# Kernel optimization log

Measured on AMD Instinct MI355X. Metric: run time of the kernel, lower is better.

## Reference

```python
import jax, jax.numpy as jnp
import numpy as np

# --- model hyperparameters (match init_kwargs / TrajectoryDecoder defaults) ---
R, T, KREG = 3, 16, 8          # num_radii, num_theta, reg_dim
RADIUS = 40.0                  # radius_scale
VEHICLE_HIDDEN = 16
MAP_HIDDEN = 8
IN_CH = VEHICLE_HIDDEN + MAP_HIDDEN  # 24
PREDICT_WINDOW = 30
TWO_PI = 2.0 * np.pi


def _reg_roll(f):
    # f: [..., C, k] -> [..., C, k(l), k(m)] with entry f[..., c, (m-l)%k]
    m = jnp.arange(KREG)[None, :]
    l = jnp.arange(KREG)[:, None]
    return f[..., (m - l) % KREG]


def _equilinear(W, f):
    # equivariant linear map between regular reps = circular (group) conv over reg dim
    # W: [out, in, k], f: [..., in, k] -> [..., out, k]
    return jnp.einsum('oil,...ilm->...om', W, _reg_roll(f))


def _reg2rho1(f, w):
    # frequency-1 Fourier projection of the regular rep -> rho1 (2-vector); 2 free params
    ang = TWO_PI * jnp.arange(KREG) / KREG
    c, s = jnp.cos(ang), jnp.sin(ang)
    W2 = jnp.stack([w[0] * c - w[1] * s, w[0] * s + w[1] * c], axis=-1)  # [k, 2]
    return jnp.einsum('...cm,md->...cd', f, W2)


def _cts_aggregate(dst_p, src_p, H, src_mask):
    # Continuous conv aggregation: bilinear interpolation of a polar-binned kernel
    # already contracted with source features.
    # H: [B, S, R, T, O, k] per-source, per-(radius,theta)-bin transformed features
    B, S, O = src_p.shape[0], src_p.shape[1], H.shape[-2]
    rel = src_p[:, None, :, :] - dst_p[:, :, None, :]      # [B, Nd, S, 2]
    d = jnp.sqrt(jnp.sum(rel * rel, axis=-1) + 1e-12)      # [B, Nd, S]
    valid = (d < RADIUS).astype(dst_p.dtype) * src_mask[:, None, :]
    win = jnp.maximum(1.0 - (d / RADIUS) ** 2, 0.0) ** 3   # CConv window
    cnt = jnp.maximum(jnp.sum(valid, axis=-1, keepdims=True), 1.0)
    base_w = valid * win / cnt
    # radial interpolation (clamped linear)
    u = jnp.clip(d / RADIUS, 0.0, 1.0) * (R - 1)
    r0f = jnp.floor(u); wr = u - r0f
    r0 = r0f.astype(jnp.int32); r1 = jnp.minimum(r0 + 1, R - 1)
    # angular interpolation (circular linear)
    t = ((jnp.arctan2(rel[..., 1], rel[..., 0]) / TWO_PI) % 1.0) * T
    t0f = jnp.floor(t); wt = t - t0f
    t0 = t0f.astype(jnp.int32) % T; t1 = (t0 + 1) % T
    Hf = H.reshape(B, S, R * T, O, KREG)
    bidx = jnp.arange(B)[:, None, None]
    sidx = jnp.arange(S)[None, None, :]
    out = jnp.zeros((B, dst_p.shape[1], O, KREG), dtype=dst_p.dtype)
    for ri, ti, cw in ((r0, t0, (1 - wr) * (1 - wt)),
                       (r0, t1, (1 - wr) * wt),
                       (r1, t0, wr * (1 - wt)),
                       (r1, t1, wr * wt)):
        g = Hf[bidx, sidx, ri * T + ti]                    # [B, Nd, S, O, k] irregular gather
        out = out + jnp.einsum('bns,bnsok->bnok', base_w * cw, g)
    return out


def _conv_reg(K, src_p, dst_p, f, src_mask):
    # EquiCtsConv2dRegToReg: per-bin group conv over reg dim, then continuous-conv gather
    H = jnp.einsum('rtoil,bsilm->bsrtom', K, _reg_roll(f))
    return _cts_aggregate(dst_p, src_p, H, src_mask)


def _conv_rho1(K, src_p, dst_p, v, src_mask):
    # EquiCtsConv2dRho1ToReg (in_channels=1): contract 2-vector input per bin
    H = jnp.einsum('rtomd,bsd->bsrtom', K, v)
    return _cts_aggregate(dst_p, src_p, H, src_mask)


def _decode(p, feat, car_mask, K_vehicle, Wd_vehicle, K_conv1, Wd1, K_conv2, Wd2):
    out = _conv_reg(K_vehicle, p, p, feat, car_mask) + _equilinear(Wd_vehicle, feat)
    for K, Wd in ((K_conv1, Wd1), (K_conv2, Wd2)):
        inf = jax.nn.relu(out)
        oc = _conv_reg(K, p, p, inf, car_mask)
        od = _equilinear(Wd, inf)
        out = oc + od + out if od.shape[-2] == out.shape[-2] else oc + od
    return jax.nn.relu(out)


def _forward(p, feat, map_p, map_feat, car_mask, map_mask,
             K_vehicle, Wd_vehicle, K_conv1, Wd1, K_conv2, Wd2,
             Wd_back, w_rho1, K_map):
    outputs = []
    output = _decode(p, feat, car_mask, K_vehicle, Wd_vehicle, K_conv1, Wd1, K_conv2, Wd2)
    delta = _reg2rho1(output, w_rho1)                      # [B, N, 3, 2]
    outputs.append(delta.at[..., 0, :].add(p))
    for _ in range(1, PREDICT_WINDOW):
        p = p + delta[..., 0, :]
        back = jnp.tanh(_equilinear(Wd_back, output))      # [B, N, 16, k]
        feat_v = feat[..., :VEHICLE_HIDDEN, :] * back
        enc = jax.nn.relu(_conv_rho1(K_map, map_p, p, map_feat, map_mask))  # MapEncoder
        feat = jnp.concatenate([feat_v, enc], axis=-2)     # [B, N, 24, k]
        output = _decode(p, feat, car_mask, K_vehicle, Wd_vehicle, K_conv1, Wd1, K_conv2, Wd2)
        delta = _reg2rho1(output, w_rho1)
        outputs.append(delta.at[..., 0, :].add(p))
    return jnp.stack(outputs, axis=0)                      # [30, B, N, 3, 2]


def setup_inputs() -> dict:
    key = jax.random.key(0)
    ks = jax.random.split(key, 13)
    B, N, M = 8, 64, 1024
    sc = 0.1
    return {
        'p': jax.random.normal(ks[0], (B, N, 2)) * 20.0,
        'feat': jax.random.normal(ks[1], (B, N, IN_CH, KREG)),
        'map_p': jax.random.normal(ks[2], (B, M, 2)) * 20.0,
        'map_feat': jax.random.normal(ks[3], (B, M, 2)),
        'car_mask': jnp.ones((B, N), dtype=jnp.float32),
        'map_mask': jnp.ones((B, M), dtype=jnp.float32),
        'K_vehicle': jax.random.normal(ks[4], (R, T, 8, IN_CH, KREG)) * sc,
        'Wd_vehicle': jax.random.normal(ks[5], (8, IN_CH, KREG)) * sc,
        'K_conv1': jax.random.normal(ks[6], (R, T, 8, 8, KREG)) * sc,
        'Wd1': jax.random.normal(ks[7], (8, 8, KREG)) * sc,
        'K_conv2': jax.random.normal(ks[8], (R, T, 3, 8, KREG)) * sc,
        'Wd2': jax.random.normal(ks[9], (3, 8, KREG)) * sc,
        'Wd_back': jax.random.normal(ks[10], (VEHICLE_HIDDEN, 3, KREG)) * sc,
        'w_rho1': jax.random.normal(ks[11], (2,)) * sc,
        'K_map': jax.random.normal(ks[12], (R, T, MAP_HIDDEN, KREG, 2)) * sc,
    }


def reference(p, feat, map_p, map_feat, car_mask, map_mask,
              K_vehicle, Wd_vehicle, K_conv1, Wd1, K_conv2, Wd2,
              Wd_back, w_rho1, K_map):
    return _forward(p, feat, map_p, map_feat, car_mask, map_mask,
                    K_vehicle, Wd_vehicle, K_conv1, Wd1, K_conv2, Wd2,
                    Wd_back, w_rho1, K_map)
```

## Files before the change

kernel.cpp:

```cpp
#include <hip/hip_runtime.h>
#include <math.h>

#define NB 8
#define NV 64
#define NM 1024
#define NR 3
#define NT 16
#define KR 8
#define RTOT 48
#define RADIUSF 40.0f
#define TWO_PIF 6.283185307179586f

__device__ __forceinline__ unsigned int pack_bf16x2(float a, float b) {
    unsigned int ua = __float_as_uint(a), ub = __float_as_uint(b);
    ua = (ua + 0x7FFFu + ((ua >> 16) & 1u)) >> 16;
    ub = (ub + 0x7FFFu + ((ub >> 16) & 1u)) & 0xFFFF0000u;
    return ua | ub;
}
__device__ __forceinline__ float2 unpack_bf16x2(unsigned int u) {
    float2 r;
    r.x = __uint_as_float(u << 16);
    r.y = __uint_as_float(u & 0xFFFF0000u);
    return r;
}

__device__ __forceinline__ float fast_atan2(float y, float x) {
    float ax = fabsf(x), ay = fabsf(y);
    float mx = fmaxf(ax, ay), mn = fminf(ax, ay);
    float z = mn / fmaxf(mx, 1e-30f);
    float z2 = z * z;
    float r = fmaf(z2, fmaf(z2, fmaf(z2, fmaf(z2, 0.0208351f, -0.0851330f),
                                     0.1801410f), -0.3302995f), 0.9998660f) * z;
    r = (ay > ax) ? (1.57079637f - r) : r;
    r = (x < 0.f) ? (3.14159274f - r) : r;
    return (y < 0.f) ? -r : r;
}

__device__ __forceinline__ void pair_geom(float relx, float rely, float mask,
                                          float& valid, float& win,
                                          int bin[4], float cw[4]) {
    float d = sqrtf(relx * relx + rely * rely + 1e-12f);
    valid = (d < RADIUSF) ? mask : 0.0f;
    float q = d * (1.0f / RADIUSF);
    float w1 = fmaxf(1.0f - q * q, 0.0f);
    win = w1 * w1 * w1;
    float u = fminf(fmaxf(q, 0.0f), 1.0f) * (float)(NR - 1);
    float r0f = floorf(u);
    float wr = u - r0f;
    int r0 = (int)r0f;
    int r1 = min(r0 + 1, NR - 1);
    float a = fast_atan2(rely, relx) * (1.0f / TWO_PIF);
    a = a - floorf(a);
    float t = a * (float)NT;
    float t0f = floorf(t);
    float wt = t - t0f;
    int t0 = ((int)t0f) & (NT - 1);
    int t1 = (t0 + 1) & (NT - 1);
    bin[0] = r0 * NT + t0; cw[0] = (1.0f - wr) * (1.0f - wt);
    bin[1] = r0 * NT + t1; cw[1] = (1.0f - wr) * wt;
    bin[2] = r1 * NT + t0; cw[2] = wr * (1.0f - wt);
    bin[3] = r1 * NT + t1; cw[3] = wr * wt;
}

__global__ __launch_bounds__(256) void k_trans(
        const float* __restrict__ Kv, const float* __restrict__ K1g,
        const float* __restrict__ K2g, float4* __restrict__ KTv,
        float4* __restrict__ KT1, float4* __restrict__ KT2) {
    int idx = blockIdx.x * 256 + threadIdx.x;
    if (idx < 48 * 384) {
        int j = idx / 384, p = idx % 384;
        KTv[idx] = *(const float4*)(Kv + p * 192 + j * 4);
    } else if (idx < 48 * 384 + 16 * 384) {
        int r = idx - 48 * 384;
        int j = r / 384, p = r % 384;
        KT1[r] = *(const float4*)(K1g + p * 64 + j * 4);
    } else if (idx < 48 * 384 + 16 * 384 + 16 * 144) {
        int r = idx - (48 * 384 + 16 * 384);
        int j = r / 144, p = r % 144;
        KT2[r] = *(const float4*)(K2g + p * 64 + j * 4);
    }
}

template<int ICH, int NPAIR, int OCH, int ROWLEN>
__device__ __forceinline__ void h_phase(int tid, int bn, const float* s_f,
        const float4* __restrict__ KT, unsigned short* __restrict__ Hb) {
    for (int pp = tid; pp < NPAIR; pp += 256) {
        float acc[KR];
#pragma unroll
        for (int m = 0; m < KR; ++m) acc[m] = 0.f;
#pragma unroll 8
        for (int i = 0; i < ICH; ++i) {
            float4 k0 = KT[(2 * i) * NPAIR + pp];
            float4 k1 = KT[(2 * i + 1) * NPAIR + pp];
            float kk[8] = {k0.x, k0.y, k0.z, k0.w, k1.x, k1.y, k1.z, k1.w};
            float ff[8];
            *(float4*)&ff[0] = *(const float4*)&s_f[i * 8];
            *(float4*)&ff[4] = *(const float4*)&s_f[i * 8 + 4];
#pragma unroll
            for (int l = 0; l < KR; ++l) {
                float kl = kk[l];
#pragma unroll
                for (int m = 0; m < KR; ++m)
                    acc[m] = fmaf(kl, ff[(m - l) & 7], acc[m]);
            }
        }
        int rt = pp / OCH, o = pp - rt * OCH;
        uint4 u;
        u.x = pack_bf16x2(acc[0], acc[1]);
        u.y = pack_bf16x2(acc[2], acc[3]);
        u.z = pack_bf16x2(acc[4], acc[5]);
        u.w = pack_bf16x2(acc[6], acc[7]);
        *(uint4*)&Hb[(size_t)(bn * RTOT + rt) * ROWLEN + o * 8] = u;
    }
}

__global__ __launch_bounds__(256) void k_H0(const float* __restrict__ inb,
        const float4* __restrict__ KT, unsigned short* __restrict__ Hb) {
    __shared__ __align__(16) float s_f[192];
    int bs = blockIdx.x, tid = threadIdx.x;
    if (tid < 192) s_f[tid] = inb[bs * 192 + tid];
    __syncthreads();
    h_phase<24, 384, 8, 64>(tid, bs, s_f, KT, Hb);
}

__device__ __forceinline__ void agg64_bf16(int tid, const float* s_w,
        const int* s_row, const unsigned short* __restrict__ Hb,
        float* s_part) {
    int w = tid >> 6, lane = tid & 63;
    int g = lane >> 3, c = lane & 7;
    float acc[8];
#pragma unroll
    for (int m = 0; m < 8; ++m) acc[m] = 0.f;
#pragma unroll
    for (int r = 0; r < 8; ++r) {
        int idx = w * 64 + r * 8 + g;
        float we = s_w[idx];
        uint4 u = *(const uint4*)&Hb[(size_t)s_row[idx] * 64 + c * 8];
        float2 q0 = unpack_bf16x2(u.x), q1 = unpack_bf16x2(u.y);
        float2 q2 = unpack_bf16x2(u.z), q3 = unpack_bf16x2(u.w);
        acc[0] = fmaf(we, q0.x, acc[0]); acc[1] = fmaf(we, q0.y, acc[1]);
        acc[2] = fmaf(we, q1.x, acc[2]); acc[3] = fmaf(we, q1.y, acc[3]);
        acc[4] = fmaf(we, q2.x, acc[4]); acc[5] = fmaf(we, q2.y, acc[5]);
        acc[6] = fmaf(we, q3.x, acc[6]); acc[7] = fmaf(we, q3.y, acc[7]);
    }
    float* pp = &s_part[(w * 8 + g) * 64 + c * 8];
#pragma unroll
    for (int m = 0; m < 8; ++m) pp[m] = acc[m];
}

__device__ __forceinline__ void agg32_bf16(int tid, const float* s_w,
        const int* s_row, const unsigned short* __restrict__ Hb,
        float* s_part) {
    int w = tid >> 6, lane = tid & 63;
    int g = lane >> 2, c = lane & 3;
    float acc[8];
#pragma unroll
    for (int m = 0; m < 8; ++m) acc[m] = 0.f;
#pragma unroll
    for (int r = 0; r < 4; ++r) {
        int idx = w * 64 + r * 16 + g;
        float we = s_w[idx];
        uint4 u = *(const uint4*)&Hb[(size_t)s_row[idx] * 32 + c * 8];
        float2 q0 = unpack_bf16x2(u.x), q1 = unpack_bf16x2(u.y);
        float2 q2 = unpack_bf16x2(u.z), q3 = unpack_bf16x2(u.w);
        acc[0] = fmaf(we, q0.x, acc[0]); acc[1] = fmaf(we, q0.y, acc[1]);
        acc[2] = fmaf(we, q1.x, acc[2]); acc[3] = fmaf(we, q1.y, acc[3]);
        acc[4] = fmaf(we, q2.x, acc[4]); acc[5] = fmaf(we, q2.y, acc[5]);
        acc[6] = fmaf(we, q3.x, acc[6]); acc[7] = fmaf(we, q3.y, acc[7]);
    }
    float* pp = &s_part[(w * 16 + g) * 32 + c * 8];
#pragma unroll
    for (int m = 0; m < 8; ++m) pp[m] = acc[m];
}

__global__ __launch_bounds__(256) void k_A1(int t,
        float* __restrict__ p, const float* __restrict__ out2buf,
        const unsigned short* __restrict__ H2b, const float* __restrict__ Wd2,
        const float* __restrict__ w4, const int* __restrict__ bin4,
        const float* __restrict__ w_rho1,
        float* __restrict__ oDbuf, float* __restrict__ out) {
    __shared__ float s_w[256];
    __shared__ int   s_row[256];
    __shared__ float s_in[64];
    __shared__ __align__(16) float s_part[64 * 32];
    __shared__ float s_oD[24];
    __shared__ float s_w2[16];
    int tid = threadIdx.x, bn = blockIdx.x, b = bn >> 6, n = bn & 63;
    float2 pold = *(const float2*)&p[bn * 2];

    s_w[tid] = w4[bn * 256 + tid];
    s_row[tid] = (b * NV + (tid >> 2)) * RTOT + bin4[bn * 256 + tid];
    if (tid < 64) s_in[tid] = out2buf[bn * 64 + tid];
    if (tid >= 224 && tid < 240) {
        int r = tid - 224, m = r >> 1, dd = r & 1;
        float ang = TWO_PIF * (float)m / (float)KR;
        float sn, cs; sincosf(ang, &sn, &cs);
        float w0 = w_rho1[0], wq = w_rho1[1];
        s_w2[r] = (dd == 0) ? (w0 * cs - wq * sn) : (w0 * sn + wq * cs);
    }
    __syncthreads();

    agg32_bf16(tid, s_w, s_row, H2b, s_part);
    __syncthreads();
    if (tid < 24) {
        float tot = 0.f;
#pragma unroll
        for (int k = 0; k < 64; ++k) tot += s_part[k * 32 + tid];
        int o = tid / KR, m = tid & 7;
#pragma unroll
        for (int i = 0; i < 8; ++i) {
            const float* Wr = Wd2 + (o * 8 + i) * KR;
#pragma unroll
            for (int l = 0; l < KR; ++l)
                tot = fmaf(Wr[l], fmaxf(s_in[i * KR + ((m - l) & 7)], 0.f), tot);
        }
        float v = fmaxf(tot, 0.f);
        s_oD[tid] = v;
        oDbuf[bn * 24 + tid] = v;
    }
    __syncthreads();

    float dx0 = 0.f, dy0 = 0.f;
#pragma unroll
    for (int m = 0; m < KR; ++m) {
        float v = s_oD[m];
        dx0 = fmaf(v, s_w2[m * 2 + 0], dx0);
        dy0 = fmaf(v, s_w2[m * 2 + 1], dy0);
    }
    if (tid < 6) {
        int c = tid >> 1, dd = tid & 1;
        float acc = 0.f;
#pragma unroll
        for (int m = 0; m < KR; ++m)
            acc = fmaf(s_oD[c * KR + m], s_w2[m * 2 + dd], acc);
        if (c == 0) acc += (dd ? pold.y : pold.x);
        out[(((t - 1) * NB + b) * NV + n) * 6 + tid] = acc;
    }
    if (tid == 0) {
        p[bn * 2 + 0] = pold.x + dx0;
        p[bn * 2 + 1] = pold.y + dy0;
    }
}

__global__ __launch_bounds__(256) void k_A2(
        const float* __restrict__ p, const float* __restrict__ oDbuf,
        float* __restrict__ feat, const float* __restrict__ WdBack,
        const float* __restrict__ Kmap, const float* __restrict__ map_p,
        const float* __restrict__ map_feat, const float* __restrict__ map_mask,
        const float4* __restrict__ KTv, unsigned short* __restrict__ Hvb) {
    __shared__ float s_oD[24];
    __shared__ float s_G4[4 * 96];
    __shared__ float s_G[96];
    __shared__ float s_wred[4];
    __shared__ __align__(16) float s_f2[192];
    int tid = threadIdx.x, bn = blockIdx.x, b = bn >> 6;

    float2 pn = *(const float2*)&p[bn * 2];
    float pdx = pn.x, pdy = pn.y;

    float2 mp[4], mf[4]; float mm[4];
#pragma unroll
    for (int j = 0; j < 4; ++j) {
        int s = tid + j * 256;
        mp[j] = *(const float2*)&map_p[(b * NM + s) * 2];
        mm[j] = map_mask[b * NM + s];
        mf[j] = *(const float2*)&map_feat[(b * NM + s) * 2];
    }
    if (tid < 24) s_oD[tid] = oDbuf[bn * 24 + tid];
    if (tid < 96) { s_G4[tid] = 0.f; s_G4[96 + tid] = 0.f; s_G4[192 + tid] = 0.f; s_G4[288 + tid] = 0.f; }
    __syncthreads();

    float lc = 0.f;
    float* myG = &s_G4[(tid >> 6) * 96];
#pragma unroll
    for (int j = 0; j < 4; ++j) {
        float valid, win; int bin[4]; float cw[4];
        pair_geom(mp[j].x - pdx, mp[j].y - pdy, mm[j], valid, win, bin, cw);
        lc += valid;
        float ww = valid * win;
        if (ww > 0.f) {
#pragma unroll
            for (int q = 0; q < 4; ++q) {
                float w = ww * cw[q];
                atomicAdd(&myG[bin[q] * 2 + 0], w * mf[j].x);
                atomicAdd(&myG[bin[q] * 2 + 1], w * mf[j].y);
            }
        }
    }
#pragma unroll
    for (int off = 32; off > 0; off >>= 1) lc += __shfl_xor(lc, off);
    if ((tid & 63) == 0) s_wred[tid >> 6] = lc;
    __syncthreads();
    if (tid < 96) s_G[tid] = s_G4[tid] + s_G4[96 + tid] + s_G4[192 + tid] + s_G4[288 + tid];
    __syncthreads();
    float invc = 1.0f / fmaxf(s_wred[0] + s_wred[1] + s_wred[2] + s_wred[3], 1.0f);

    if (tid < 64) {
        float acc = 0.f;
#pragma unroll 8
        for (int rt = 0; rt < RTOT; ++rt) {
            float2 k2 = *(const float2*)&Kmap[(rt * 64 + tid) * 2];
            acc = fmaf(k2.x, s_G[rt * 2 + 0], acc);
            acc = fmaf(k2.y, s_G[rt * 2 + 1], acc);
        }
        s_f2[128 + tid] = fmaxf(acc * invc, 0.f);
    }
    if (tid >= 128) {
        int r = tid - 128, i = r >> 3, m = r & 7;
        float acc = 0.f;
#pragma unroll
        for (int c = 0; c < 3; ++c)
#pragma unroll
            for (int l = 0; l < KR; ++l)
                acc = fmaf(WdBack[(i * 3 + c) * 8 + l], s_oD[c * 8 + ((m - l) & 7)], acc);
        s_f2[r] = feat[bn * 192 + r] * tanhf(acc);
    }
    __syncthreads();
    if (tid < 192) feat[bn * 192 + tid] = s_f2[tid];

    h_phase<24, 384, 8, 64>(tid, bn, s_f2, KTv, Hvb);
}

__global__ __launch_bounds__(256) void k_B(
        const float* __restrict__ p, const float* __restrict__ car_mask,
        const float* __restrict__ feat, const unsigned short* __restrict__ Hvb,
        const float* __restrict__ WdV,
        float* __restrict__ w4, int* __restrict__ bin4,
        const float4* __restrict__ KT1,
        float* __restrict__ out1, unsigned short* __restrict__ H1b) {
    __shared__ float s_psrc[NV * 2];
    __shared__ float s_w[256];
    __shared__ int   s_row[256];
    __shared__ __align__(16) float s_in[192];
    __shared__ __align__(16) float s_part[32 * 64];
    __shared__ __align__(16) float s_f2[64];
    int tid = threadIdx.x, bn = blockIdx.x, b = bn >> 6, n = bn & 63;
    if (tid < 128) s_psrc[tid] = p[b * 128 + tid];
    if (tid < 192) s_in[tid] = feat[bn * 192 + tid];
    __syncthreads();
    if (tid < NV) {
        int s = tid;
        float valid, win; int bin[4]; float cw[4];
        pair_geom(s_psrc[s * 2 + 0] - s_psrc[n * 2 + 0],
                  s_psrc[s * 2 + 1] - s_psrc[n * 2 + 1],
                  car_mask[b * NV + s], valid, win, bin, cw);
        float c = valid;
#pragma unroll
        for (int off = 32; off > 0; off >>= 1) c += __shfl_xor(c, off);
        float bw = valid * win / fmaxf(c, 1.0f);
#pragma unroll
        for (int q = 0; q < 4; ++q) {
            float wv = bw * cw[q];
            s_w[s * 4 + q] = wv;
            s_row[s * 4 + q] = (b * NV + s) * RTOT + bin[q];
            w4[bn * 256 + s * 4 + q] = wv;
            bin4[bn * 256 + s * 4 + q] = bin[q];
        }
    }
    __syncthreads();
    agg64_bf16(tid, s_w, s_row, Hvb, s_part);
    __syncthreads();
    if (tid < 64) {
        float tot = 0.f;
#pragma unroll
        for (int k = 0; k < 32; ++k) tot += s_part[k * 64 + tid];
        int o = tid >> 3, m = tid & 7;
#pragma unroll
        for (int i = 0; i < 24; ++i) {
            const float* Wr = WdV + (o * 24 + i) * KR;
#pragma unroll
            for (int l = 0; l < KR; ++l)
                tot = fmaf(Wr[l], s_in[i * KR + ((m - l) & 7)], tot);
        }
        out1[bn * 64 + tid] = tot;
        s_f2[tid] = fmaxf(tot, 0.f);
    }
    __syncthreads();
    h_phase<8, 384, 8, 64>(tid, bn, s_f2, KT1, H1b);
}

__global__ __launch_bounds__(256) void k_C(const float* __restrict__ out1,
        const unsigned short* __restrict__ H1b, const float* __restrict__ Wd1,
        const float* __restrict__ w4, const int* __restrict__ bin4,
        const float4* __restrict__ KT2, float* __restrict__ out2,
        unsigned short* __restrict__ H2b) {
    __shared__ float s_w[256];
    __shared__ int   s_row[256];
    __shared__ float s_in[64];
    __shared__ __align__(16) float s_part[32 * 64];
    __shared__ __align__(16) float s_f2[64];
    int tid = threadIdx.x, bn = blockIdx.x, b = bn >> 6;
    s_w[tid] = w4[bn * 256 + tid];
    s_row[tid] = (b * NV + (tid >> 2)) * RTOT + bin4[bn * 256 + tid];
    if (tid < 64) s_in[tid] = out1[bn * 64 + tid];
    __syncthreads();
    agg64_bf16(tid, s_w, s_row, H1b, s_part);
    __syncthreads();
    if (tid < 64) {
        float tot = 0.f;
#pragma unroll
        for (int k = 0; k < 32; ++k) tot += s_part[k * 64 + tid];
        int o = tid >> 3, m = tid & 7;
#pragma unroll
        for (int i = 0; i < 8; ++i) {
            const float* Wr = Wd1 + (o * 8 + i) * KR;
#pragma unroll
            for (int l = 0; l < KR; ++l)
                tot = fmaf(Wr[l], fmaxf(s_in[i * KR + ((m - l) & 7)], 0.f), tot);
        }
        tot += s_in[tid];
        out2[bn * 64 + tid] = tot;
        s_f2[tid] = fmaxf(tot, 0.f);
    }
    __syncthreads();
    h_phase<8, 144, 3, 32>(tid, bn, s_f2, KT2, H2b);
}

__global__ __launch_bounds__(256) void k_fin(
        const float* __restrict__ p, const float* __restrict__ out2buf,
        const unsigned short* __restrict__ H2b, const float* __restrict__ Wd2,
        const float* __restrict__ w4, const int* __restrict__ bin4,
        const float* __restrict__ w_rho1, float* __restrict__ out) {
    __shared__ float s_w[256];
    __shared__ int   s_row[256];
    __shared__ float s_in[64];
    __shared__ __align__(16) float s_part[64 * 32];
    __shared__ float s_oD[24];
    __shared__ float s_w2[16];
    int tid = threadIdx.x, bn = blockIdx.x, b = bn >> 6, n = bn & 63;
    s_w[tid] = w4[bn * 256 + tid];
    s_row[tid] = (b * NV + (tid >> 2)) * RTOT + bin4[bn * 256 + tid];
    if (tid < 64) s_in[tid] = out2buf[bn * 64 + tid];
    if (tid >= 224 && tid < 240) {
        int r = tid - 224, m = r >> 1, dd = r & 1;
        float ang = TWO_PIF * (float)m / (float)KR;
        float sn, cs; sincosf(ang, &sn, &cs);
        float w0 = w_rho1[0], wq = w_rho1[1];
        s_w2[r] = (dd == 0) ? (w0 * cs - wq * sn) : (w0 * sn + wq * cs);
    }
    __syncthreads();
    agg32_bf16(tid, s_w, s_row, H2b, s_part);
    __syncthreads();
    if (tid < 24) {
        float tot = 0.f;
#pragma unroll
        for (int k = 0; k < 64; ++k) tot += s_part[k * 32 + tid];
        int o = tid / KR, m = tid & 7;
#pragma unroll
        for (int i = 0; i < 8; ++i) {
            const float* Wr = Wd2 + (o * 8 + i) * KR;
#pragma unroll
            for (int l = 0; l < KR; ++l)
                tot = fmaf(Wr[l], fmaxf(s_in[i * KR + ((m - l) & 7)], 0.f), tot);
        }
        s_oD[tid] = fmaxf(tot, 0.f);
    }
    __syncthreads();
    if (tid < 6) {
        int c = tid >> 1, dd = tid & 1;
        float acc = 0.f;
#pragma unroll
        for (int m = 0; m < KR; ++m)
            acc = fmaf(s_oD[c * KR + m], s_w2[m * 2 + dd], acc);
        if (c == 0) acc += p[bn * 2 + dd];
        out[((29 * NB + b) * NV + n) * 6 + tid] = acc;
    }
}

extern "C" void kernel_launch(void* const* d_in, const int* in_sizes, int n_in,
                              void* d_out, int out_size, void* d_ws, size_t ws_size,
                              hipStream_t stream) {
    const float* in_p     = (const float*)d_in[0];
    const float* in_feat  = (const float*)d_in[1];
    const float* map_p    = (const float*)d_in[2];
    const float* map_feat = (const float*)d_in[3];
    const float* car_mask = (const float*)d_in[4];
    const float* map_mask = (const float*)d_in[5];
    const float* Kv       = (const float*)d_in[6];
    const float* WdV      = (const float*)d_in[7];
    const float* K1       = (const float*)d_in[8];
    const float* Wd1      = (const float*)d_in[9];
    const float* K2       = (const float*)d_in[10];
    const float* Wd2      = (const float*)d_in[11];
    const float* WdBack   = (const float*)d_in[12];
    const float* w_rho1   = (const float*)d_in[13];
    const float* Kmap     = (const float*)d_in[14];

    float* ws   = (float*)d_ws;
    float* pbuf  = ws;
    float* feat  = ws + 2048;
    float* out1  = ws + 100352;
    float* out2  = ws + 133120;
    float* w4    = ws + 178176;
    int*   bin4  = (int*)(ws + 309248);
    float4* KTv  = (float4*)(ws + 440320);
    float4* KT1  = (float4*)(ws + 514048);
    float4* KT2  = (float4*)(ws + 538624);
    unsigned short* Hvb = (unsigned short*)(ws + 547840);
    unsigned short* H1b = (unsigned short*)(ws + 1334272);
    unsigned short* H2b = (unsigned short*)(ws + 2120704);
    float* oDbuf = ws + 2513920;
    float* out   = (float*)d_out;

    hipMemcpyAsync(pbuf, in_p, NB * NV * 2 * sizeof(float),
                   hipMemcpyDeviceToDevice, stream);
    hipMemcpyAsync(feat, in_feat, NB * NV * 24 * KR * sizeof(float),
                   hipMemcpyDeviceToDevice, stream);

    k_trans<<<105, 256, 0, stream>>>(Kv, K1, K2, KTv, KT1, KT2);
    k_H0<<<NB * NV, 256, 0, stream>>>(feat, KTv, Hvb);

    k_B<<<NB * NV, 256, 0, stream>>>(pbuf, car_mask, feat, Hvb, WdV, w4, bin4, KT1, out1, H1b);
    k_C<<<NB * NV, 256, 0, stream>>>(out1, H1b, Wd1, w4, bin4, KT2, out2, H2b);

    for (int t = 1; t < 30; ++t) {
        k_A1<<<NB * NV, 256, 0, stream>>>(t, pbuf, out2, H2b, Wd2, w4, bin4,
                                          w_rho1, oDbuf, out);
        k_A2<<<NB * NV, 256, 0, stream>>>(pbuf, oDbuf, feat, WdBack, Kmap,
                                          map_p, map_feat, map_mask, KTv, Hvb);
        k_B<<<NB * NV, 256, 0, stream>>>(pbuf, car_mask, feat, Hvb, WdV, w4, bin4, KT1, out1, H1b);
        k_C<<<NB * NV, 256, 0, stream>>>(out1, H1b, Wd1, w4, bin4, KT2, out2, H2b);
    }
    k_fin<<<NB * NV, 256, 0, stream>>>(pbuf, out2, H2b, Wd2, w4, bin4, w_rho1, out);
}
```

Before: 1.656 ms.

## Fuse per-step decode kernels and widen blocks to 1024 threads with shuffle reductions

Merges the two per-timestep kernels, position update/output and map aggregation plus H recompute, into one kernel. This removes one launch per step and the oDbuf round trip through global memory. All per-step kernels move to 1024-thread blocks, so each thread handles one map point, and the h_phase loop spreads its 384 pairs across more threads. The gather-aggregation reductions now use wavefront butterfly shuffles instead of large shared-memory partial buffers. The trade-off is lower occupancy per CU with 1024-thread blocks, many idle threads in some phases, and more shuffle instructions.

After: 2.020 ms. 1.22x slower.

```diff
diff --git a/kernel.cpp b/kernel.cpp
--- a/kernel.cpp
+++ b/kernel.cpp
@@ -81,10 +81,10 @@
     }
 }
 
-template<int ICH, int NPAIR, int OCH, int ROWLEN>
+template<int ICH, int NPAIR, int OCH, int ROWLEN, int STRIDE>
 __device__ __forceinline__ void h_phase(int tid, int bn, const float* s_f,
         const float4* __restrict__ KT, unsigned short* __restrict__ Hb) {
-    for (int pp = tid; pp < NPAIR; pp += 256) {
+    for (int pp = tid; pp < NPAIR; pp += STRIDE) {
         float acc[KR];
 #pragma unroll
         for (int m = 0; m < KR; ++m) acc[m] = 0.f;
@@ -114,98 +114,87 @@
     }
 }
 
+__device__ __forceinline__ void bfly8(float acc[8]) {
+#pragma unroll
+    for (int off = 1; off < 64; off <<= 1) {
+#pragma unroll
+        for (int j = 0; j < 8; ++j) acc[j] += __shfl_xor(acc[j], off);
+    }
+}
+
 __global__ __launch_bounds__(256) void k_H0(const float* __restrict__ inb,
         const float4* __restrict__ KT, unsigned short* __restrict__ Hb) {
     __shared__ __align__(16) float s_f[192];
     int bs = blockIdx.x, tid = threadIdx.x;
     if (tid < 192) s_f[tid] = inb[bs * 192 + tid];
     __syncthreads();
-    h_phase<24, 384, 8, 64>(tid, bs, s_f, KT, Hb);
-}
-
-__device__ __forceinline__ void agg64_bf16(int tid, const float* s_w,
-        const int* s_row, const unsigned short* __restrict__ Hb,
-        float* s_part) {
-    int w = tid >> 6, lane = tid & 63;
-    int g = lane >> 3, c = lane & 7;
-    float acc[8];
-#pragma unroll
-    for (int m = 0; m < 8; ++m) acc[m] = 0.f;
-#pragma unroll
-    for (int r = 0; r < 8; ++r) {
-        int idx = w * 64 + r * 8 + g;
-        float we = s_w[idx];
-        uint4 u = *(const uint4*)&Hb[(size_t)s_row[idx] * 64 + c * 8];
-        float2 q0 = unpack_bf16x2(u.x), q1 = unpack_bf16x2(u.y);
-        float2 q2 = unpack_bf16x2(u.z), q3 = unpack_bf16x2(u.w);
-        acc[0] = fmaf(we, q0.x, acc[0]); acc[1] = fmaf(we, q0.y, acc[1]);
-        acc[2] = fmaf(we, q1.x, acc[2]); acc[3] = fmaf(we, q1.y, acc[3]);
-        acc[4] = fmaf(we, q2.x, acc[4]); acc[5] = fmaf(we, q2.y, acc[5]);
-        acc[6] = fmaf(we, q3.x, acc[6]); acc[7] = fmaf(we, q3.y, acc[7]);
-    }
-    float* pp = &s_part[(w * 8 + g) * 64 + c * 8];
-#pragma unroll
-    for (int m = 0; m < 8; ++m) pp[m] = acc[m];
-}
-
-__device__ __forceinline__ void agg32_bf16(int tid, const float* s_w,
-        const int* s_row, const unsigned short* __restrict__ Hb,
-        float* s_part) {
-    int w = tid >> 6, lane = tid & 63;
-    int g = lane >> 2, c = lane & 3;
-    float acc[8];
-#pragma unroll
-    for (int m = 0; m < 8; ++m) acc[m] = 0.f;
-#pragma unroll
-    for (int r = 0; r < 4; ++r) {
-        int idx = w * 64 + r * 16 + g;
-        float we = s_w[idx];
-        uint4 u = *(const uint4*)&Hb[(size_t)s_row[idx] * 32 + c * 8];
-        float2 q0 = unpack_bf16x2(u.x), q1 = unpack_bf16x2(u.y);
-        float2 q2 = unpack_bf16x2(u.z), q3 = unpack_bf16x2(u.w);
-        acc[0] = fmaf(we, q0.x, acc[0]); acc[1] = fmaf(we, q0.y, acc[1]);
-        acc[2] = fmaf(we, q1.x, acc[2]); acc[3] = fmaf(we, q1.y, acc[3]);
-        acc[4] = fmaf(we, q2.x, acc[4]); acc[5] = fmaf(we, q2.y, acc[5]);
-        acc[6] = fmaf(we, q3.x, acc[6]); acc[7] = fmaf(we, q3.y, acc[7]);
-    }
-    float* pp = &s_part[(w * 16 + g) * 32 + c * 8];
-#pragma unroll
-    for (int m = 0; m < 8; ++m) pp[m] = acc[m];
-}
-
-__global__ __launch_bounds__(256) void k_A1(int t,
+    h_phase<24, 384, 8, 64, 256>(tid, bs, s_f, KT, Hb);
+}
+
+__global__ __launch_bounds__(1024) void k_AM(int t,
         float* __restrict__ p, const float* __restrict__ out2buf,
         const unsigned short* __restrict__ H2b, const float* __restrict__ Wd2,
         const float* __restrict__ w4, const int* __restrict__ bin4,
-        const float* __restrict__ w_rho1,
-        float* __restrict__ oDbuf, float* __restrict__ out) {
+        const float* __restrict__ w_rho1, float* __restrict__ feat,
+        const float* __restrict__ WdBack, const float* __restrict__ Kmap,
+        const float* __restrict__ map_p, const float* __restrict__ map_feat,
+        const float* __restrict__ map_mask,
+        const float4* __restrict__ KTv, unsigned short* __restrict__ Hvb,
+        float* __restrict__ out) {
     __shared__ float s_w[256];
     __shared__ int   s_row[256];
     __shared__ float s_in[64];
-    __shared__ __align__(16) float s_part[64 * 32];
+    __shared__ float s_p2[16 * 8];
     __shared__ float s_oD[24];
     __shared__ float s_w2[16];
+    __shared__ float s_G16[16 * 96];
+    __shared__ float s_G[96];
+    __shared__ float s_wred[16];
+    __shared__ __align__(16) float s_f2[192];
+
     int tid = threadIdx.x, bn = blockIdx.x, b = bn >> 6, n = bn & 63;
+    int w = tid >> 6, lane = tid & 63;
     float2 pold = *(const float2*)&p[bn * 2];
 
-    s_w[tid] = w4[bn * 256 + tid];
-    s_row[tid] = (b * NV + (tid >> 2)) * RTOT + bin4[bn * 256 + tid];
-    if (tid < 64) s_in[tid] = out2buf[bn * 64 + tid];
-    if (tid >= 224 && tid < 240) {
-        int r = tid - 224, m = r >> 1, dd = r & 1;
+    float2 mp = *(const float2*)&map_p[(b * NM + tid) * 2];
+    float  mm = map_mask[b * NM + tid];
+    float2 mf = *(const float2*)&map_feat[(b * NM + tid) * 2];
+
+    if (tid < 256) {
+        s_w[tid] = w4[bn * 256 + tid];
+        s_row[tid] = (b * NV + (tid >> 2)) * RTOT + bin4[bn * 256 + tid];
+    }
+    if (tid >= 256 && tid < 320) s_in[tid - 256] = out2buf[bn * 64 + (tid - 256)];
+    if (tid >= 320 && tid < 336) {
+        int r = tid - 320, m = r >> 1, dd = r & 1;
         float ang = TWO_PIF * (float)m / (float)KR;
         float sn, cs; sincosf(ang, &sn, &cs);
         float w0 = w_rho1[0], wq = w_rho1[1];
         s_w2[r] = (dd == 0) ? (w0 * cs - wq * sn) : (w0 * sn + wq * cs);
     }
-    __syncthreads();
-
-    agg32_bf16(tid, s_w, s_row, H2b, s_part);
+    for (int i = tid; i < 16 * 96; i += 1024) s_G16[i] = 0.f;
+    __syncthreads();
+
+    {
+        int cgrp = w >> 2, esub = w & 3;
+        int e = esub * 64 + lane;
+        float we = s_w[e];
+        uint4 u = *(const uint4*)&H2b[(size_t)s_row[e] * 32 + cgrp * 8];
+        float2 q0 = unpack_bf16x2(u.x), q1 = unpack_bf16x2(u.y);
+        float2 q2 = unpack_bf16x2(u.z), q3 = unpack_bf16x2(u.w);
+        float acc[8] = {we * q0.x, we * q0.y, we * q1.x, we * q1.y,
+                        we * q2.x, we * q2.y, we * q3.x, we * q3.y};
+        bfly8(acc);
+        if (lane == 0) {
+#pragma unroll
+            for (int j = 0; j < 8; ++j) s_p2[w * 8 + j] = acc[j];
+        }
+    }
     __syncthreads();
     if (tid < 24) {
-        float tot = 0.f;
-#pragma unroll
-        for (int k = 0; k < 64; ++k) tot += s_part[k * 32 + tid];
+        int cgrp = tid >> 3, j = tid & 7;
+        float tot = s_p2[(cgrp * 4 + 0) * 8 + j] + s_p2[(cgrp * 4 + 1) * 8 + j]
+                  + s_p2[(cgrp * 4 + 2) * 8 + j] + s_p2[(cgrp * 4 + 3) * 8 + j];
         int o = tid / KR, m = tid & 7;
 #pragma unroll
         for (int i = 0; i < 8; ++i) {
@@ -214,9 +203,7 @@
             for (int l = 0; l < KR; ++l)
                 tot = fmaf(Wr[l], fmaxf(s_in[i * KR + ((m - l) & 7)], 0.f), tot);
         }
-        float v = fmaxf(tot, 0.f);
-        s_oD[tid] = v;
-        oDbuf[bn * 24 + tid] = v;
+        s_oD[tid] = fmaxf(tot, 0.f);
     }
     __syncthreads();
 
@@ -236,66 +223,42 @@
         if (c == 0) acc += (dd ? pold.y : pold.x);
         out[(((t - 1) * NB + b) * NV + n) * 6 + tid] = acc;
     }
-    if (tid == 0) {
-        p[bn * 2 + 0] = pold.x + dx0;
-        p[bn * 2 + 1] = pold.y + dy0;
-    }
-}
-
-__global__ __launch_bounds__(256) void k_A2(
-        const float* __restrict__ p, const float* __restrict__ oDbuf,
-        float* __restrict__ feat, const float* __restrict__ WdBack,
-        const float* __restrict__ Kmap, const float* __restrict__ map_p,
-        const float* __restrict__ map_feat, const float* __restrict__ map_mask,
-        const float4* __restrict__ KTv, unsigned short* __restrict__ Hvb) {
-    __shared__ float s_oD[24];
-    __shared__ float s_G4[4 * 96];
-    __shared__ float s_G[96];
-    __shared__ float s_wred[4];
-    __shared__ __align__(16) float s_f2[192];
-    int tid = threadIdx.x, bn = blockIdx.x, b = bn >> 6;
-
-    float2 pn = *(const float2*)&p[bn * 2];
-    float pdx = pn.x, pdy = pn.y;
-
-    float2 mp[4], mf[4]; float mm[4];
-#pragma unroll
-    for (int j = 0; j < 4; ++j) {
-        int s = tid + j * 256;
-        mp[j] = *(const float2*)&map_p[(b * NM + s) * 2];
-        mm[j] = map_mask[b * NM + s];
-        mf[j] = *(const float2*)&map_feat[(b * NM + s) * 2];
-    }
-    if (tid < 24) s_oD[tid] = oDbuf[bn * 24 + tid];
-    if (tid < 96) { s_G4[tid] = 0.f; s_G4[96 + tid] = 0.f; s_G4[192 + tid] = 0.f; s_G4[288 + tid] = 0.f; }
-    __syncthreads();
-
-    float lc = 0.f;
-    float* myG = &s_G4[(tid >> 6) * 96];
-#pragma unroll
-    for (int j = 0; j < 4; ++j) {
+    float pdx = pold.x + dx0, pdy = pold.y + dy0;
+    if (tid == 0) { p[bn * 2 + 0] = pdx; p[bn * 2 + 1] = pdy; }
+
+    float lc;
+    {
         float valid, win; int bin[4]; float cw[4];
-        pair_geom(mp[j].x - pdx, mp[j].y - pdy, mm[j], valid, win, bin, cw);
-        lc += valid;
+        pair_geom(mp.x - pdx, mp.y - pdy, mm, valid, win, bin, cw);
+        lc = valid;
         float ww = valid * win;
+        float* myG = &s_G16[w * 96];
         if (ww > 0.f) {
 #pragma unroll
             for (int q = 0; q < 4; ++q) {
-                float w = ww * cw[q];
-                atomicAdd(&myG[bin[q] * 2 + 0], w * mf[j].x);
-                atomicAdd(&myG[bin[q] * 2 + 1], w * mf[j].y);
+                float wq_ = ww * cw[q];
+                atomicAdd(&myG[bin[q] * 2 + 0], wq_ * mf.x);
+                atomicAdd(&myG[bin[q] * 2 + 1], wq_ * mf.y);
             }
         }
     }
 #pragma unroll
-    for (int off = 32; off > 0; off >>= 1) lc += __shfl_xor(lc, off);
-    if ((tid & 63) == 0) s_wred[tid >> 6] = lc;
-    __syncthreads();
-    if (tid < 96) s_G[tid] = s_G4[tid] + s_G4[96 + tid] + s_G4[192 + tid] + s_G4[288 + tid];
-    __syncthreads();
-    float invc = 1.0f / fmaxf(s_wred[0] + s_wred[1] + s_wred[2] + s_wred[3], 1.0f);
+    for (int off = 1; off < 64; off <<= 1) lc += __shfl_xor(lc, off);
+    if (lane == 0) s_wred[w] = lc;
+    __syncthreads();
+    if (tid < 96) {
+        float g = 0.f;
+#pragma unroll
+        for (int c = 0; c < 16; ++c) g += s_G16[c * 96 + tid];
+        s_G[tid] = g;
+    }
+    __syncthreads();
 
     if (tid < 64) {
+        float cnt = 0.f;
+#pragma unroll
+        for (int c = 0; c < 16; ++c) cnt += s_wred[c];
+        float invc = 1.0f / fmaxf(cnt, 1.0f);
         float acc = 0.f;
 #pragma unroll 8
         for (int rt = 0; rt < RTOT; ++rt) {
@@ -305,7 +268,7 @@
         }
         s_f2[128 + tid] = fmaxf(acc * invc, 0.f);
     }
-    if (tid >= 128) {
+    if (tid >= 128 && tid < 256) {
         int r = tid - 128, i = r >> 3, m = r & 7;
         float acc = 0.f;
 #pragma unroll
@@ -318,10 +281,10 @@
     __syncthreads();
     if (tid < 192) feat[bn * 192 + tid] = s_f2[tid];
 
-    h_phase<24, 384, 8, 64>(tid, bn, s_f2, KTv, Hvb);
-}
-
-__global__ __launch_bounds__(256) void k_B(
+    h_phase<24, 384, 8, 64, 1024>(tid, bn, s_f2, KTv, Hvb);
+}
+
+__global__ __launch_bounds__(1024) void k_B(
         const float* __restrict__ p, const float* __restrict__ car_mask,
         const float* __restrict__ feat, const unsigned short* __restrict__ Hvb,
         const float* __restrict__ WdV,
@@ -332,11 +295,12 @@
     __shared__ float s_w[256];
     __shared__ int   s_row[256];
     __shared__ __align__(16) float s_in[192];
-    __shared__ __align__(16) float s_part[32 * 64];
+    __shared__ float s_p[16 * 8];
     __shared__ __align__(16) float s_f2[64];
     int tid = threadIdx.x, bn = blockIdx.x, b = bn >> 6, n = bn & 63;
+    int w = tid >> 6, lane = tid & 63;
     if (tid < 128) s_psrc[tid] = p[b * 128 + tid];
-    if (tid < 192) s_in[tid] = feat[bn * 192 + tid];
+    if (tid >= 256 && tid < 448) s_in[tid - 256] = feat[bn * 192 + (tid - 256)];
     __syncthreads();
     if (tid < NV) {
         int s = tid;
@@ -358,12 +322,33 @@
         }
     }
     __syncthreads();
-    agg64_bf16(tid, s_w, s_row, Hvb, s_part);
+    {
+        int cgrp = w >> 1, esub = w & 1;
+        int e0 = esub * 128 + lane, e1 = e0 + 64;
+        float we0 = s_w[e0], we1 = s_w[e1];
+        uint4 u0 = *(const uint4*)&Hvb[(size_t)s_row[e0] * 64 + cgrp * 8];
+        uint4 u1 = *(const uint4*)&Hvb[(size_t)s_row[e1] * 64 + cgrp * 8];
+        float acc[8];
+        {
+            float2 a0 = unpack_bf16x2(u0.x), a1 = unpack_bf16x2(u0.y);
+            float2 a2 = unpack_bf16x2(u0.z), a3 = unpack_bf16x2(u0.w);
+            float2 b0 = unpack_bf16x2(u1.x), b1 = unpack_bf16x2(u1.y);
+            float2 b2 = unpack_bf16x2(u1.z), b3 = unpack_bf16x2(u1.w);
+            acc[0] = we0 * a0.x + we1 * b0.x; acc[1] = we0 * a0.y + we1 * b0.y;
+            acc[2] = we0 * a1.x + we1 * b1.x; acc[3] = we0 * a1.y + we1 * b1.y;
+            acc[4] = we0 * a2.x + we1 * b2.x; acc[5] = we0 * a2.y + we1 * b2.y;
+            acc[6] = we0 * a3.x + we1 * b3.x; acc[7] = we0 * a3.y + we1 * b3.y;
+        }
+        bfly8(acc);
+        if (lane == 0) {
+#pragma unroll
+            for (int j = 0; j < 8; ++j) s_p[w * 8 + j] = acc[j];
+        }
+    }
     __syncthreads();
     if (tid < 64) {
-        float tot = 0.f;
-#pragma unroll
-        for (int k = 0; k < 32; ++k) tot += s_part[k * 64 + tid];
+        int cgrp = tid >> 3, j = tid & 7;
+        float tot = s_p[(cgrp * 2 + 0) * 8 + j] + s_p[(cgrp * 2 + 1) * 8 + j];
         int o = tid >> 3, m = tid & 7;
 #pragma unroll
         for (int i = 0; i < 24; ++i) {
@@ -376,10 +361,10 @@
         s_f2[tid] = fmaxf(tot, 0.f);
     }
     __syncthreads();
-    h_phase<8, 384, 8, 64>(tid, bn, s_f2, KT1, H1b);
-}
-
-__global__ __launch_bounds__(256) void k_C(const float* __restrict__ out1,
+    h_phase<8, 384, 8, 64, 1024>(tid, bn, s_f2, KT1, H1b);
+}
+
+__global__ __launch_bounds__(1024) void k_C(const float* __restrict__ out1,
         const unsigned short* __restrict__ H1b, const float* __restrict__ Wd1,
         const float* __restrict__ w4, const int* __restrict__ bin4,
         const float4* __restrict__ KT2, float* __restrict__ out2,
@@ -387,19 +372,43 @@
     __shared__ float s_w[256];
     __shared__ int   s_row[256];
     __shared__ float s_in[64];
-    __shared__ __align__(16) float s_part[32 * 64];
+    __shared__ float s_p[16 * 8];
     __shared__ __align__(16) float s_f2[64];
     int tid = threadIdx.x, bn = blockIdx.x, b = bn >> 6;
-    s_w[tid] = w4[bn * 256 + tid];
-    s_row[tid] = (b * NV + (tid >> 2)) * RTOT + bin4[bn * 256 + tid];
-    if (tid < 64) s_in[tid] = out1[bn * 64 + tid];
-    __syncthreads();
-    agg64_bf16(tid, s_w, s_row, H1b, s_part);
+    int w = tid >> 6, lane = tid & 63;
+    if (tid < 256) {
+        s_w[tid] = w4[bn * 256 + tid];
+        s_row[tid] = (b * NV + (tid >> 2)) * RTOT + bin4[bn * 256 + tid];
+    }
+    if (tid >= 256 && tid < 320) s_in[tid - 256] = out1[bn * 64 + (tid - 256)];
+    __syncthreads();
+    {
+        int cgrp = w >> 1, esub = w & 1;
+        int e0 = esub * 128 + lane, e1 = e0 + 64;
+        float we0 = s_w[e0], we1 = s_w[e1];
+        uint4 u0 = *(const uint4*)&H1b[(size_t)s_row[e0] * 64 + cgrp * 8];
+        uint4 u1 = *(const uint4*)&H1b[(size_t)s_row[e1] * 64 + cgrp * 8];
+        float acc[8];
+        {
+            float2 a0 = unpack_bf16x2(u0.x), a1 = unpack_bf16x2(u0.y);
+            float2 a2 = unpack_bf16x2(u0.z), a3 = unpack_bf16x2(u0.w);
+            float2 b0 = unpack_bf16x2(u1.x), b1 = unpack_bf16x2(u1.y);
+            float2 b2 = unpack_bf16x2(u1.z), b3 = unpack_bf16x2(u1.w);
+            acc[0] = we0 * a0.x + we1 * b0.x; acc[1] = we0 * a0.y + we1 * b0.y;
+            acc[2] = we0 * a1.x + we1 * b1.x; acc[3] = we0 * a1.y + we1 * b1.y;
+            acc[4] = we0 * a2.x + we1 * b2.x; acc[5] = we0 * a2.y + we1 * b2.y;
+            acc[6] = we0 * a3.x + we1 * b3.x; acc[7] = we0 * a3.y + we1 * b3.y;
+        }
+        bfly8(acc);
+        if (lane == 0) {
+#pragma unroll
+            for (int j = 0; j < 8; ++j) s_p[w * 8 + j] = acc[j];
+        }
+    }
     __syncthreads();
     if (tid < 64) {
-        float tot = 0.f;
-#pragma unroll
-        for (int k = 0; k < 32; ++k) tot += s_part[k * 64 + tid];
+        int cgrp = tid >> 3, j = tid & 7;
+        float tot = s_p[(cgrp * 2 + 0) * 8 + j] + s_p[(cgrp * 2 + 1) * 8 + j];
         int o = tid >> 3, m = tid & 7;
 #pragma unroll
         for (int i = 0; i < 8; ++i) {
@@ -413,10 +422,10 @@
         s_f2[tid] = fmaxf(tot, 0.f);
     }
     __syncthreads();
-    h_phase<8, 144, 3, 32>(tid, bn, s_f2, KT2, H2b);
-}
-
-__global__ __launch_bounds__(256) void k_fin(
+    h_phase<8, 144, 3, 32, 1024>(tid, bn, s_f2, KT2, H2b);
+}
+
+__global__ __launch_bounds__(1024) void k_fin(
         const float* __restrict__ p, const float* __restrict__ out2buf,
         const unsigned short* __restrict__ H2b, const float* __restrict__ Wd2,
         const float* __restrict__ w4, const int* __restrict__ bin4,
@@ -424,27 +433,44 @@
     __shared__ float s_w[256];
     __shared__ int   s_row[256];
     __shared__ float s_in[64];
-    __shared__ __align__(16) float s_part[64 * 32];
+    __shared__ float s_p2[16 * 8];
     __shared__ float s_oD[24];
     __shared__ float s_w2[16];
     int tid = threadIdx.x, bn = blockIdx.x, b = bn >> 6, n = bn & 63;
-    s_w[tid] = w4[bn * 256 + tid];
-    s_row[tid] = (b * NV + (tid >> 2)) * RTOT + bin4[bn * 256 + tid];
-    if (tid < 64) s_in[tid] = out2buf[bn * 64 + tid];
-    if (tid >= 224 && tid < 240) {
-        int r = tid - 224, m = r >> 1, dd = r & 1;
+    int w = tid >> 6, lane = tid & 63;
+    if (tid < 256) {
+        s_w[tid] = w4[bn * 256 + tid];
+        s_row[tid] = (b * NV + (tid >> 2)) * RTOT + bin4[bn * 256 + tid];
+    }
+    if (tid >= 256 && tid < 320) s_in[tid - 256] = out2buf[bn * 64 + (tid - 256)];
+    if (tid >= 320 && tid < 336) {
+        int r = tid - 320, m = r >> 1, dd = r & 1;
         float ang = TWO_PIF * (float)m / (float)KR;
         float sn, cs; sincosf(ang, &sn, &cs);
         float w0 = w_rho1[0], wq = w_rho1[1];
         s_w2[r] = (dd == 0) ? (w0 * cs - wq * sn) : (w0 * sn + wq * cs);
     }
     __syncthreads();
-    agg32_bf16(tid, s_w, s_row, H2b, s_part);
+    {
+        int cgrp = w >> 2, esub = w & 3;
+        int e = esub * 64 + lane;
+        float we = s_w[e];
+        uint4 u = *(const uint4*)&H2b[(size_t)s_row[e] * 32 + cgrp * 8];
+        float2 q0 = unpack_bf16x2(u.x), q1 = unpack_bf16x2(u.y);
+        float2 q2 = unpack_bf16x2(u.z), q3 = unpack_bf16x2(u.w);
+        float acc[8] = {we * q0.x, we * q0.y, we * q1.x, we * q1.y,
+                        we * q2.x, we * q2.y, we * q3.x, we * q3.y};
+        bfly8(acc);
+        if (lane == 0) {
+#pragma unroll
+            for (int j = 0; j < 8; ++j) s_p2[w * 8 + j] = acc[j];
+        }
+    }
     __syncthreads();
     if (tid < 24) {
-        float tot = 0.f;
-#pragma unroll
-        for (int k = 0; k < 64; ++k) tot += s_part[k * 32 + tid];
+        int cgrp = tid >> 3, j = tid & 7;
+        float tot = s_p2[(cgrp * 4 + 0) * 8 + j] + s_p2[(cgrp * 4 + 1) * 8 + j]
+                  + s_p2[(cgrp * 4 + 2) * 8 + j] + s_p2[(cgrp * 4 + 3) * 8 + j];
         int o = tid / KR, m = tid & 7;
 #pragma unroll
         for (int i = 0; i < 8; ++i) {
@@ -499,7 +525,6 @@
     unsigned short* Hvb = (unsigned short*)(ws + 547840);
     unsigned short* H1b = (unsigned short*)(ws + 1334272);
     unsigned short* H2b = (unsigned short*)(ws + 2120704);
-    float* oDbuf = ws + 2513920;
     float* out   = (float*)d_out;
 
     hipMemcpyAsync(pbuf, in_p, NB * NV * 2 * sizeof(float),
@@ -510,16 +535,15 @@
     k_trans<<<105, 256, 0, stream>>>(Kv, K1, K2, KTv, KT1, KT2);
     k_H0<<<NB * NV, 256, 0, stream>>>(feat, KTv, Hvb);
 
-    k_B<<<NB * NV, 256, 0, stream>>>(pbuf, car_mask, feat, Hvb, WdV, w4, bin4, KT1, out1, H1b);
-    k_C<<<NB * NV, 256, 0, stream>>>(out1, H1b, Wd1, w4, bin4, KT2, out2, H2b);
+    k_B<<<NB * NV, 1024, 0, stream>>>(pbuf, car_mask, feat, Hvb, WdV, w4, bin4, KT1, out1, H1b);
+    k_C<<<NB * NV, 1024, 0, stream>>>(out1, H1b, Wd1, w4, bin4, KT2, out2, H2b);
 
     for (int t = 1; t < 30; ++t) {
-        k_A1<<<NB * NV, 256, 0, stream>>>(t, pbuf, out2, H2b, Wd2, w4, bin4,
-                                          w_rho1, oDbuf, out);
-        k_A2<<<NB * NV, 256, 0, stream>>>(pbuf, oDbuf, feat, WdBack, Kmap,
-                                          map_p, map_feat, map_mask, KTv, Hvb);
-        k_B<<<NB * NV, 256, 0, stream>>>(pbuf, car_mask, feat, Hvb, WdV, w4, bin4, KT1, out1, H1b);
-        k_C<<<NB * NV, 256, 0, stream>>>(out1, H1b, Wd1, w4, bin4, KT2, out2, H2b);
-    }
-    k_fin<<<NB * NV, 256, 0, stream>>>(pbuf, out2, H2b, Wd2, w4, bin4, w_rho1, out);
-}
+        k_AM<<<NB * NV, 1024, 0, stream>>>(t, pbuf, out2, H2b, Wd2, w4, bin4,
+                                           w_rho1, feat, WdBack, Kmap, map_p,
+                                           map_feat, map_mask, KTv, Hvb, out);
+        k_B<<<NB * NV, 1024, 0, stream>>>(pbuf, car_mask, feat, Hvb, WdV, w4, bin4, KT1, out1, H1b);
+        k_C<<<NB * NV, 1024, 0, stream>>>(out1, H1b, Wd1, w4, bin4, KT2, out2, H2b);
+    }
+    k_fin<<<NB * NV, 1024, 0, stream>>>(pbuf, out2, H2b, Wd2, w4, bin4, w_rho1, out);
+}
```
